# Performance work log

Hardware: AMD Instinct MI355X
Metric: run time of the kernel (lower is better)

Reference implementation:

```python
import jax, jax.numpy as jnp
import numpy as np
import math

B, S, D = 32, 2048, 1024


def setup_inputs() -> dict:
    key = jax.random.key(0)
    ks = jax.random.split(key, 8)
    x = jax.random.normal(ks[0], (B, S, D), dtype=jnp.float32)
    # right-padding mask: True = padding, each row has a random valid length in [S//2, S]
    lengths = jax.random.randint(ks[1], (B, 1), S // 2, S + 1)
    attention_mask = jnp.arange(S)[None, :] >= lengths  # [B, S] bool
    scale = 1.0 / math.sqrt(D)
    gate_w1 = jax.random.normal(ks[2], (D, D // 2), dtype=jnp.float32) * scale
    gate_b1 = jnp.zeros((D // 2,), dtype=jnp.float32)
    gate_w2 = jax.random.normal(ks[3], (D // 2, 1), dtype=jnp.float32) * scale
    gate_b2 = jnp.zeros((1,), dtype=jnp.float32)
    decay_lambda = jnp.float32(0.05)
    attention_query = jax.random.normal(ks[4], (D,), dtype=jnp.float32)
    key_w = jax.random.normal(ks[5], (D, D), dtype=jnp.float32) * scale
    key_b = jnp.zeros((D,), dtype=jnp.float32)
    return {
        "utterance_embeddings": x,
        "attention_mask": attention_mask,
        "gate_w1": gate_w1, "gate_b1": gate_b1,
        "gate_w2": gate_w2, "gate_b2": gate_b2,
        "decay_lambda": decay_lambda,
        "attention_query": attention_query,
        "key_w": key_w, "key_b": key_b,
    }


def reference(utterance_embeddings, attention_mask, gate_w1, gate_b1, gate_w2,
              gate_b2, decay_lambda, attention_query, key_w, key_b):
    x = utterance_embeddings  # [B, S, D]
    bsz, seq_len, dim = x.shape
    # suppression gate: Linear -> GELU(exact) -> Linear -> Sigmoid, output [B, S, 1]
    h = jax.nn.gelu(jnp.einsum('bsd,dk->bsk', x, gate_w1) + gate_b1, approximate=False)
    gate = jax.nn.sigmoid(jnp.einsum('bsk,ko->bso', h, gate_w2) + gate_b2)
    gated = x * gate  # [B, S, D]
    keys = jnp.einsum('bsd,de->bse', gated, key_w) + key_b  # [B, S, D]
    logits = jnp.einsum('d,bsd->bs', attention_query, keys) / jnp.sqrt(jnp.float32(dim))
    t_idx = jnp.arange(seq_len, dtype=jnp.float32)[None, :]  # [1, S]
    valid_lengths = jnp.sum(~attention_mask, axis=1, keepdims=True).astype(jnp.float32)
    penalty_idx = jnp.maximum(valid_lengths - 1.0 - t_idx, 0.0)  # [B, S]
    pos_lambda = jax.nn.softplus(decay_lambda)
    decayed = logits - pos_lambda * penalty_idx
    decayed = jnp.where(attention_mask, jnp.float32(-10000.0), decayed)
    alpha = jax.nn.softmax(decayed, axis=1)  # [B, S]
    scene_vector = jnp.einsum('bs,bsd->bd', alpha, gated)  # [B, D]
    return scene_vector
```

## Files before the change

kernel.cpp:

```cpp
#include <hip/hip_runtime.h>
#include <hip/hip_bf16.h>
#include <math.h>

#define BQ 32
#define SQ 2048
#define DQ 1024
#define NQ 512
#define MQ (BQ*SQ)
#define BM 128
#define BN 256
#define BK 32

typedef __attribute__((ext_vector_type(8))) short bf16x8;
typedef __attribute__((ext_vector_type(4))) float f32x4;

#define SB0 __builtin_amdgcn_sched_barrier(0)

__device__ __forceinline__ short f2bf(float f){
  return __builtin_bit_cast(short, __float2bfloat16(f));
}

__device__ __forceinline__ void gload_lds16(const void* g, void* l){
  __builtin_amdgcn_global_load_lds(
      (const __attribute__((address_space(1))) unsigned int*)g,
      (__attribute__((address_space(3))) unsigned int*)l, 16, 0, 0);
}

__global__ void k_w1t(const float* __restrict__ w1, short* __restrict__ w1t){
  int i = blockIdx.x*256 + threadIdx.x;
  if (i >= NQ*DQ) return;
  int n = i >> 10, k = i & (DQ-1);
  w1t[i] = f2bf(w1[(size_t)k*NQ + n]);
}

__global__ void k_wq(const float* __restrict__ kw, const float* __restrict__ kb,
                     const float* __restrict__ q, float* __restrict__ wq){
  __shared__ float sh[4];
  int d = blockIdx.x, t = threadIdx.x;
  const float* row = (d < DQ) ? (kw + (size_t)d*DQ) : kb;
  float s = 0.f;
  for (int e=t;e<DQ;e+=256) s += row[e]*q[e];
  #pragma unroll
  for (int o=32;o;o>>=1) s += __shfl_down(s,o);
  if ((t&63)==0) sh[t>>6]=s;
  __syncthreads();
  if (t==0) wq[d] = sh[0]+sh[1]+sh[2]+sh[3];
}

__global__ void k_det(const unsigned int* __restrict__ m, int* __restrict__ flag){
  __shared__ int so, sf;
  int t = threadIdx.x;
  if (t==0){ so=0; sf=0; }
  __syncthreads();
  int o=0, f1=0;
  for (int i=t;i<MQ/4;i+=256){
    unsigned v = m[i];
    if (v==0x3F800000u) f1=1;
    else if (v>1u) o=1;
  }
  if (o) atomicOr(&so,1);
  if (f1) atomicOr(&sf,1);
  __syncthreads();
  if (t==0) *flag = so?2:(sf?1:0);
}

__global__ __launch_bounds__(256) void k_len(const void* __restrict__ maskp,
                                             const int* __restrict__ flag,
                                             int* __restrict__ lens){
  __shared__ int sh[4];
  int b = blockIdx.x, t = threadIdx.x;
  int fl = *flag;
  const unsigned char* m8 = (const unsigned char*)maskp;
  const float* mf = (const float*)maskp;
  const int* mi = (const int*)maskp;
  int cnt = 0;
  #pragma unroll
  for (int i=0;i<8;i++){
    size_t idx = (size_t)b*SQ + t + i*256;
    int mm = (fl==2) ? (m8[idx]!=0) : (fl==1) ? (mf[idx]!=0.0f) : (mi[idx]!=0);
    cnt += mm^1;
  }
  #pragma unroll
  for (int o=32;o;o>>=1) cnt += __shfl_down(cnt,o);
  if ((t&63)==0) sh[t>>6]=cnt;
  __syncthreads();
  if (t==0) lens[b] = sh[0]+sh[1]+sh[2]+sh[3];
}

__global__ __launch_bounds__(512) void k_gate(
    const float* __restrict__ x, const short* __restrict__ w1t,
    const float* __restrict__ wq, const float* __restrict__ w2,
    const float* __restrict__ b1,
    float* __restrict__ gpart, float* __restrict__ xqv)
{
  __shared__ __align__(16) short As[2][BM*BK];
  __shared__ __align__(16) short Bs[3][BN*BK];
  __shared__ float wqs[DQ];
  __shared__ float red[4][BM];

  int tid = threadIdx.x;
  int phys = blockIdx.x;
  int bid = ((phys & 7) << 7) | (phys >> 3);
  int bm = bid >> 1, bn = bid & 1;
  int m0 = bm*BM, n0 = bn*BN;
  int lane = tid & 63, wid = tid >> 6;
  int wm = wid >> 2, wn = wid & 3;
  int lo = lane & 15, hi = lane >> 4;

  wqs[tid]     = wq[tid];
  wqs[tid+512] = wq[tid+512];

  int ar = tid >> 2, acf = (tid & 3) * 8;
  const float* asrc = x + (size_t)(m0 + ar)*DQ + acf;
  const short* bsrc = w1t + (size_t)(n0 + (tid>>2))*DQ + (tid&3)*8;

  float w2v[4], b1v[4];
  #pragma unroll
  for (int fn=0;fn<4;fn++){
    int n = n0 + wn*64 + fn*16 + lo;
    w2v[fn] = w2[n]; b1v[fn] = b1[n];
  }

  gload_lds16(bsrc,                       &Bs[0][tid*8]);
  gload_lds16(bsrc + (size_t)128*DQ,      &Bs[0][4096 + tid*8]);
  gload_lds16(bsrc + BK,                  &Bs[1][tid*8]);
  gload_lds16(bsrc + (size_t)128*DQ + BK, &Bs[1][4096 + tid*8]);
  f32x4 a0 = *(const f32x4*)(asrc);
  f32x4 a1 = *(const f32x4*)(asrc + 4);
  {
    bf16x8 sv;
    #pragma unroll
    for (int j=0;j<4;j++){ sv[j]=f2bf(a0[j]); sv[4+j]=f2bf(a1[j]); }
    *(bf16x8*)(&As[0][ar*BK + acf]) = sv;
  }
  asm volatile("s_waitcnt lgkmcnt(0)" ::: "memory");
  SB0;
  __builtin_amdgcn_s_barrier();
  SB0;
  float xqacc = 0.f;
  if (bn == 0){
    f32x4 w0 = *(const f32x4*)(wqs + acf);
    f32x4 w1f = *(const f32x4*)(wqs + acf + 4);
    #pragma unroll
    for (int j=0;j<4;j++) xqacc += a0[j]*w0[j] + a1[j]*w1f[j];
  }

  f32x4 acc[4][4];
  #pragma unroll
  for (int a=0;a<4;a++)
    #pragma unroll
    for (int b=0;b<4;b++) acc[a][b] = (f32x4){0.f,0.f,0.f,0.f};

  f32x4 na0, na1;
  for (int t=0; t<32; ++t){
    int curA = t & 1;
    int curB = t % 3;
    if (t < 31){
      na0 = *(const f32x4*)(asrc + (t+1)*BK);
      na1 = *(const f32x4*)(asrc + (t+1)*BK + 4);
    }
    SB0;
    if (t < 30){
      int nb = (t+2) % 3;
      const short* bk = bsrc + (t+2)*BK;
      gload_lds16(bk,                  &Bs[nb][tid*8]);
      gload_lds16(bk + (size_t)128*DQ, &Bs[nb][4096 + tid*8]);
    }
    SB0;
    bf16x8 af[4], bfr[4];
    #pragma unroll
    for (int fm=0;fm<4;fm++)
      af[fm] = *(const bf16x8*)(&As[curA][(wm*64+fm*16+lo)*BK + hi*8]);
    #pragma unroll
    for (int fn=0;fn<4;fn++){
      int r = wn*64 + fn*16 + lo;
      bfr[fn] = *(const bf16x8*)(&Bs[curB][(r>>7)*4096 + (r&127)*32 + hi*8]);
    }
    #pragma unroll
    for (int fm=0;fm<4;fm++)
      #pragma unroll
      for (int fn=0;fn<4;fn++)
        acc[fm][fn] = __builtin_amdgcn_mfma_f32_16x16x32_bf16(af[fm], bfr[fn], acc[fm][fn], 0,0,0);
    SB0;
    if (t < 31){
      if (bn == 0){
        f32x4 w0 = *(const f32x4*)(wqs + (t+1)*BK + acf);
        f32x4 w1f = *(const f32x4*)(wqs + (t+1)*BK + acf + 4);
        #pragma unroll
        for (int j=0;j<4;j++) xqacc += na0[j]*w0[j] + na1[j]*w1f[j];
      }
      bf16x8 sv;
      #pragma unroll
      for (int j=0;j<4;j++){ sv[j]=f2bf(na0[j]); sv[4+j]=f2bf(na1[j]); }
      *(bf16x8*)(&As[curA^1][ar*BK + acf]) = sv;
    }
    asm volatile("s_waitcnt lgkmcnt(0)" ::: "memory");
    SB0;
    __builtin_amdgcn_s_barrier();
    SB0;
  }

  if (bn == 0){
    float s = xqacc;
    s += __shfl_xor(s,1); s += __shfl_xor(s,2);
    if ((tid & 3) == 0) xqv[m0 + ar] = s;
  }

  #pragma unroll
  for (int fm=0;fm<4;fm++){
    #pragma unroll
    for (int j=0;j<4;j++){
      float s = 0.f;
      #pragma unroll
      for (int fn=0;fn<4;fn++){
        float h = acc[fm][fn][j] + b1v[fn];
        float g = 0.5f*h*(1.0f + erff(h*0.70710678118f));
        s += g*w2v[fn];
      }
      s += __shfl_xor(s,1); s += __shfl_xor(s,2);
      s += __shfl_xor(s,4); s += __shfl_xor(s,8);
      if (lo == 0) red[wn][wm*64 + fm*16 + hi*4 + j] = s;
    }
  }
  __syncthreads();
  if (tid < BM){
    float g = red[0][tid] + red[1][tid] + red[2][tid] + red[3][tid];
    gpart[(size_t)bn*MQ + m0 + tid] = g;
  }
}

__global__ __launch_bounds__(256) void k_wpool(
    const float* __restrict__ x, const float* __restrict__ gpart,
    const float* __restrict__ xqv, const float* __restrict__ wq,
    const float* __restrict__ b2p, const float* __restrict__ lamp,
    const void* __restrict__ maskp, const int* __restrict__ flag,
    const int* __restrict__ lens,
    float* __restrict__ part, float* __restrict__ wsumv)
{
  __shared__ float wrow[256];
  __shared__ float ssum[4];
  int blk = blockIdx.x, t = threadIdx.x;
  int batch = blk >> 3;
  int sBase = (blk & 7) * 256;
  size_t R0 = (size_t)blk * 256;
  {
    size_t r = R0 + t;
    float gsum = b2p[0] + gpart[r] + gpart[(size_t)MQ + r];
    float gate = 1.0f/(1.0f+expf(-gsum));
    float qb = wq[DQ];
    float lg = (gate*xqv[r] + qb)*0.03125f;
    float lam = lamp[0];
    float posl = fmaxf(lam,0.f) + log1pf(expf(-fabsf(lam)));
    int L = lens[batch];
    int s = sBase + t;
    float pen = fmaxf((float)L - 1.0f - (float)s, 0.0f);
    int fl = *flag;
    size_t mi_ = (size_t)batch*SQ + s;
    int mm = (fl==2) ? (((const unsigned char*)maskp)[mi_]!=0)
           : (fl==1) ? (((const float*)maskp)[mi_]!=0.0f)
                     : (((const int*)maskp)[mi_]!=0);
    float e = mm ? 0.0f : expf(lg - posl*pen);
    wrow[t] = e*gate;
    float ts = e;
    #pragma unroll
    for (int o=1;o<64;o<<=1) ts += __shfl_xor(ts,o);
    if ((t&63)==0) ssum[t>>6] = ts;
  }
  __syncthreads();
  if (t==0) wsumv[blk] = ssum[0]+ssum[1]+ssum[2]+ssum[3];

  int d0 = t*4;
  const float* xb = x + R0*DQ + d0;
  f32x4 a = {0.f,0.f,0.f,0.f};
  #pragma unroll 8
  for (int s=0;s<256;s++){
    float w = wrow[s];
    f32x4 v = *(const f32x4*)(xb + (size_t)s*DQ);
    a[0] += w*v[0]; a[1] += w*v[1]; a[2] += w*v[2]; a[3] += w*v[3];
  }
  *(f32x4*)(part + (size_t)blk*DQ + d0) = a;
}

__global__ __launch_bounds__(256) void k_fin(const float* __restrict__ part,
                                             const float* __restrict__ wsumv,
                                             float* __restrict__ out){
  int i = blockIdx.x*256 + threadIdx.x;
  int b = i >> 10, d = i & 1023;
  float den = 0.f;
  #pragma unroll
  for (int c=0;c<8;c++) den += wsumv[b*8+c];
  float s = 0.f;
  #pragma unroll
  for (int c=0;c<8;c++) s += part[((size_t)(b*8+c))*DQ + d];
  out[i] = s/den;
}

extern "C" void kernel_launch(void* const* d_in, const int* in_sizes, int n_in,
                              void* d_out, int out_size, void* d_ws, size_t ws_size,
                              hipStream_t stream)
{
  const float* x    = (const float*)d_in[0];
  const void*  mask = d_in[1];
  const float* w1   = (const float*)d_in[2];
  const float* b1   = (const float*)d_in[3];
  const float* w2   = (const float*)d_in[4];
  const float* b2   = (const float*)d_in[5];
  const float* lam  = (const float*)d_in[6];
  const float* q    = (const float*)d_in[7];
  const float* kw   = (const float*)d_in[8];
  const float* kb   = (const float*)d_in[9];
  char* ws = (char*)d_ws;
  short* w1t   = (short*)ws;
  float* wq    = (float*)(ws + (1<<20));
  int*   flag  = (int*)(ws + (1<<20) + 8192);
  int*   lens  = (int*)(ws + (1<<20) + 8448);
  float* wsumv = (float*)(ws + (1<<20) + 12544);
  float* xqv   = (float*)(ws + (1<<20) + 32768);
  float* gpart = (float*)(ws + (2<<20));
  float* part  = (float*)(ws + (3<<20));
  float* out   = (float*)d_out;

  k_w1t<<<dim3((NQ*DQ+255)/256), 256, 0, stream>>>(w1, w1t);
  k_wq<<<dim3(DQ+1), 256, 0, stream>>>(kw, kb, q, wq);
  k_det<<<dim3(1), 256, 0, stream>>>((const unsigned int*)mask, flag);
  k_len<<<dim3(BQ), 256, 0, stream>>>(mask, flag, lens);
  k_gate<<<dim3((MQ/BM)*(NQ/BN)), 512, 0, stream>>>(x, w1t, wq, w2, b1,
                                                    gpart, xqv);
  k_wpool<<<dim3(MQ/256), 256, 0, stream>>>(x, gpart, xqv, wq, b2, lam,
                                            mask, flag, lens, part, wsumv);
  k_fin<<<dim3((BQ*DQ)/256), 256, 0, stream>>>(part, wsumv, out);
}
```

Measured before the change: 187.1 us.

## Simplify gate GEMM to double buffering and write per-warp gate partials

The gate GEMM's W1 tile staging drops from a triple-buffered LDS ring, prefetched two steps ahead, to a double buffer prefetched one step ahead. The hand-placed sched_barrier and lgkmcnt waits are replaced by plain __syncthreads. The LDS cross-warp reduction of the GELU·w2 partials is removed. Each warp column now writes its own partial to global memory, 8 slices in place of 2, and the pooling kernel sums all 8. This cuts LDS usage and an epilogue barrier, but the prefetch has less distance to hide global-load latency, and the gate partial buffer traffic grows.

```diff
diff --git a/kernel.cpp b/kernel.cpp
--- a/kernel.cpp
+++ b/kernel.cpp
@@ -13,8 +13,6 @@
 
 typedef __attribute__((ext_vector_type(8))) short bf16x8;
 typedef __attribute__((ext_vector_type(4))) float f32x4;
-
-#define SB0 __builtin_amdgcn_sched_barrier(0)
 
 __device__ __forceinline__ short f2bf(float f){
   return __builtin_bit_cast(short, __float2bfloat16(f));
@@ -91,18 +89,17 @@
     const float* __restrict__ x, const short* __restrict__ w1t,
     const float* __restrict__ wq, const float* __restrict__ w2,
     const float* __restrict__ b1,
-    float* __restrict__ gpart, float* __restrict__ xqv)
+    float* __restrict__ gpart, float* __restrict__ xq)
 {
   __shared__ __align__(16) short As[2][BM*BK];
-  __shared__ __align__(16) short Bs[3][BN*BK];
+  __shared__ __align__(16) short Bs[2][BN*BK];
   __shared__ float wqs[DQ];
-  __shared__ float red[4][BM];
 
   int tid = threadIdx.x;
   int phys = blockIdx.x;
   int bid = ((phys & 7) << 7) | (phys >> 3);
   int bm = bid >> 1, bn = bid & 1;
-  int m0 = bm*BM, n0 = bn*BN;
+  int m0 = bm*BM;
   int lane = tid & 63, wid = tid >> 6;
   int wm = wid >> 2, wn = wid & 3;
   int lo = lane & 15, hi = lane >> 4;
@@ -110,40 +107,37 @@
   wqs[tid]     = wq[tid];
   wqs[tid+512] = wq[tid+512];
 
-  int ar = tid >> 2, acf = (tid & 3) * 8;
-  const float* asrc = x + (size_t)(m0 + ar)*DQ + acf;
-  const short* bsrc = w1t + (size_t)(n0 + (tid>>2))*DQ + (tid&3)*8;
+  int ar = tid >> 2, ac = (tid & 3) * 8;
+  const float* asrc = x + (size_t)(m0 + ar)*DQ + ac;
+  const short* bsrc = w1t + (size_t)(bn*BN + (tid>>2))*DQ + (tid&3)*8;
 
   float w2v[4], b1v[4];
   #pragma unroll
   for (int fn=0;fn<4;fn++){
-    int n = n0 + wn*64 + fn*16 + lo;
+    int n = bn*BN + wn*64 + fn*16 + lo;
     w2v[fn] = w2[n]; b1v[fn] = b1[n];
   }
 
-  gload_lds16(bsrc,                       &Bs[0][tid*8]);
-  gload_lds16(bsrc + (size_t)128*DQ,      &Bs[0][4096 + tid*8]);
-  gload_lds16(bsrc + BK,                  &Bs[1][tid*8]);
-  gload_lds16(bsrc + (size_t)128*DQ + BK, &Bs[1][4096 + tid*8]);
-  f32x4 a0 = *(const f32x4*)(asrc);
-  f32x4 a1 = *(const f32x4*)(asrc + 4);
+  f32x4 r0 = *(const f32x4*)(asrc);
+  f32x4 r1 = *(const f32x4*)(asrc + 4);
+  gload_lds16(bsrc,                    &Bs[0][tid*8]);
+  gload_lds16(bsrc + (size_t)128*DQ,   &Bs[0][tid*8 + 4096]);
+  __syncthreads();
+  float xqacc = 0.f;
   {
-    bf16x8 sv;
-    #pragma unroll
-    for (int j=0;j<4;j++){ sv[j]=f2bf(a0[j]); sv[4+j]=f2bf(a1[j]); }
-    *(bf16x8*)(&As[0][ar*BK + acf]) = sv;
-  }
-  asm volatile("s_waitcnt lgkmcnt(0)" ::: "memory");
-  SB0;
-  __builtin_amdgcn_s_barrier();
-  SB0;
-  float xqacc = 0.f;
-  if (bn == 0){
-    f32x4 w0 = *(const f32x4*)(wqs + acf);
-    f32x4 w1f = *(const f32x4*)(wqs + acf + 4);
-    #pragma unroll
-    for (int j=0;j<4;j++) xqacc += a0[j]*w0[j] + a1[j]*w1f[j];
-  }
+    if (bn == 0){
+      f32x4 w0 = *(const f32x4*)(wqs + ac);
+      f32x4 w1v = *(const f32x4*)(wqs + ac + 4);
+      #pragma unroll
+      for (int j=0;j<4;j++)
+        xqacc += r0[j]*w0[j] + r1[j]*w1v[j];
+    }
+    bf16x8 s0;
+    #pragma unroll
+    for (int j=0;j<4;j++){ s0[j]=f2bf(r0[j]); s0[4+j]=f2bf(r1[j]); }
+    *(bf16x8*)(&As[0][ar*BK + ac]) = s0;
+  }
+  __syncthreads();
 
   f32x4 acc[4][4];
   #pragma unroll
@@ -151,59 +145,48 @@
     #pragma unroll
     for (int b=0;b<4;b++) acc[a][b] = (f32x4){0.f,0.f,0.f,0.f};
 
-  f32x4 na0, na1;
-  for (int t=0; t<32; ++t){
-    int curA = t & 1;
-    int curB = t % 3;
+  for (int t=0;t<32;t++){
+    int cur = t & 1, nxt = cur ^ 1;
+    int k0n = (t+1)*BK;
     if (t < 31){
-      na0 = *(const f32x4*)(asrc + (t+1)*BK);
-      na1 = *(const f32x4*)(asrc + (t+1)*BK + 4);
+      r0 = *(const f32x4*)(asrc + k0n);
+      r1 = *(const f32x4*)(asrc + k0n + 4);
+      gload_lds16(bsrc + k0n,                  &Bs[nxt][tid*8]);
+      gload_lds16(bsrc + (size_t)128*DQ + k0n, &Bs[nxt][tid*8 + 4096]);
     }
-    SB0;
-    if (t < 30){
-      int nb = (t+2) % 3;
-      const short* bk = bsrc + (t+2)*BK;
-      gload_lds16(bk,                  &Bs[nb][tid*8]);
-      gload_lds16(bk + (size_t)128*DQ, &Bs[nb][4096 + tid*8]);
-    }
-    SB0;
     bf16x8 af[4], bfr[4];
     #pragma unroll
     for (int fm=0;fm<4;fm++)
-      af[fm] = *(const bf16x8*)(&As[curA][(wm*64+fm*16+lo)*BK + hi*8]);
-    #pragma unroll
-    for (int fn=0;fn<4;fn++){
-      int r = wn*64 + fn*16 + lo;
-      bfr[fn] = *(const bf16x8*)(&Bs[curB][(r>>7)*4096 + (r&127)*32 + hi*8]);
-    }
+      af[fm] = *(const bf16x8*)(&As[cur][(wm*64+fm*16+lo)*BK + hi*8]);
+    #pragma unroll
+    for (int fn=0;fn<4;fn++)
+      bfr[fn] = *(const bf16x8*)(&Bs[cur][(wn*64+fn*16+lo)*BK + hi*8]);
     #pragma unroll
     for (int fm=0;fm<4;fm++)
       #pragma unroll
       for (int fn=0;fn<4;fn++)
         acc[fm][fn] = __builtin_amdgcn_mfma_f32_16x16x32_bf16(af[fm], bfr[fn], acc[fm][fn], 0,0,0);
-    SB0;
     if (t < 31){
       if (bn == 0){
-        f32x4 w0 = *(const f32x4*)(wqs + (t+1)*BK + acf);
-        f32x4 w1f = *(const f32x4*)(wqs + (t+1)*BK + acf + 4);
+        f32x4 w0 = *(const f32x4*)(wqs + k0n + ac);
+        f32x4 w1v = *(const f32x4*)(wqs + k0n + ac + 4);
         #pragma unroll
-        for (int j=0;j<4;j++) xqacc += na0[j]*w0[j] + na1[j]*w1f[j];
+        for (int j=0;j<4;j++)
+          xqacc += r0[j]*w0[j] + r1[j]*w1v[j];
       }
-      bf16x8 sv;
+      bf16x8 s0;
       #pragma unroll
-      for (int j=0;j<4;j++){ sv[j]=f2bf(na0[j]); sv[4+j]=f2bf(na1[j]); }
-      *(bf16x8*)(&As[curA^1][ar*BK + acf]) = sv;
+      for (int j=0;j<4;j++){ s0[j]=f2bf(r0[j]); s0[4+j]=f2bf(r1[j]); }
+      *(bf16x8*)(&As[nxt][ar*BK + ac]) = s0;
     }
-    asm volatile("s_waitcnt lgkmcnt(0)" ::: "memory");
-    SB0;
-    __builtin_amdgcn_s_barrier();
-    SB0;
+    __syncthreads();
   }
 
   if (bn == 0){
     float s = xqacc;
-    s += __shfl_xor(s,1); s += __shfl_xor(s,2);
-    if ((tid & 3) == 0) xqv[m0 + ar] = s;
+    s += __shfl_xor(s, 1);
+    s += __shfl_xor(s, 2);
+    if ((tid & 3) == 0) xq[m0 + ar] = s;
   }
 
   #pragma unroll
@@ -219,13 +202,11 @@
       }
       s += __shfl_xor(s,1); s += __shfl_xor(s,2);
       s += __shfl_xor(s,4); s += __shfl_xor(s,8);
-      if (lo == 0) red[wn][wm*64 + fm*16 + hi*4 + j] = s;
+      if (lo == 0){
+        int p = bn*4 + wn;
+        gpart[(size_t)p*MQ + m0 + wm*64 + fm*16 + hi*4 + j] = s;
+      }
     }
-  }
-  __syncthreads();
-  if (tid < BM){
-    float g = red[0][tid] + red[1][tid] + red[2][tid] + red[3][tid];
-    gpart[(size_t)bn*MQ + m0 + tid] = g;
   }
 }
 
@@ -245,7 +226,9 @@
   size_t R0 = (size_t)blk * 256;
   {
     size_t r = R0 + t;
-    float gsum = b2p[0] + gpart[r] + gpart[(size_t)MQ + r];
+    float gsum = b2p[0];
+    #pragma unroll
+    for (int p=0;p<8;p++) gsum += gpart[(size_t)p*MQ + r];
     float gate = 1.0f/(1.0f+expf(-gsum));
     float qb = wq[DQ];
     float lg = (gate*xqv[r] + qb)*0.03125f;
@@ -317,7 +300,7 @@
   float* wsumv = (float*)(ws + (1<<20) + 12544);
   float* xqv   = (float*)(ws + (1<<20) + 32768);
   float* gpart = (float*)(ws + (2<<20));
-  float* part  = (float*)(ws + (3<<20));
+  float* part  = (float*)(ws + (4<<20));
   float* out   = (float*)d_out;
 
   k_w1t<<<dim3((NQ*DQ+255)/256), 256, 0, stream>>>(w1, w1t);
```

Measured after the change: 186.0 us. Within noise of the previous version (-0.6%).
